# Kernel optimization log

Hardware: AMD Instinct MI355X
Metric: run time of the kernel (lower is better)

The kernel has to match this reference:

```python
import jax, jax.numpy as jnp
import numpy as np

B, S, H = 32, 1024, 768          # batch, seq_len, bert hidden
E, W, P = 128, 8, 512            # entities/sample, span width, rel pairs/sample
NT, NR = 5, 9                    # entity types, relation types
D1, HEADS1, D2, RD = 128, 2, 64, 32
REL_IN = 2 * D2 + RD + H         # 928


def _layernorm(x, g, b):
    m = x.mean(-1, keepdims=True)
    v = x.var(-1, keepdims=True)
    return (x - m) * jax.lax.rsqrt(v + 1e-5) * g + b


def _gat_dense(x, Wm, a_src, a_dst, bias, concat):
    # Fully-connected entity graph (incl. self-loops, PyG GATConv default).
    Bn, En, _ = x.shape
    Hh, D = a_src.shape
    h = (x @ Wm).reshape(Bn, En, Hh, D)                      # [B,E,h,D]
    s = jnp.einsum('behd,hd->beh', h, a_src)                 # source score
    d = jnp.einsum('behd,hd->beh', h, a_dst)                 # target score
    # edge j->i : e_ij = leaky_relu(s_j + d_i)
    e = jax.nn.leaky_relu(d[:, :, None, :] + s[:, None, :, :], 0.2)  # [B,i,j,h]
    alpha = jax.nn.softmax(e, axis=2)
    o = jnp.einsum('bijh,bjhd->bihd', alpha, h)
    o = o.reshape(Bn, En, Hh * D) if concat else o.mean(axis=2)
    return o + bias


def setup_inputs() -> dict:
    key = jax.random.key(0)
    ks = jax.random.split(key, 20)
    f = lambda k, shape: jax.random.normal(k, shape, jnp.float32) * 0.02
    return dict(
        sequence_output=jax.random.normal(ks[0], (B, S, H), jnp.float32),
        entity_starts=jax.random.randint(ks[1], (B, E), 0, S - W),
        entity_type_ids=jax.random.randint(ks[2], (B, E), 0, NT),
        pair_idx=jax.random.randint(ks[3], (B, P, 2), 0, E),
        rel_type_ids=jax.random.randint(ks[4], (B, P), 0, NR),
        entity_type_emb=f(ks[5], (NT, H)),
        rel_type_emb=f(ks[6], (NR, RD)),
        W1=f(ks[7], (H, HEADS1 * D1)), a_src1=f(ks[8], (HEADS1, D1)),
        a_dst1=f(ks[9], (HEADS1, D1)), b1=jnp.zeros((HEADS1 * D1,), jnp.float32),
        ln1_g=jnp.ones((HEADS1 * D1,), jnp.float32), ln1_b=jnp.zeros((HEADS1 * D1,), jnp.float32),
        W2=f(ks[10], (HEADS1 * D1, D2)), a_src2=f(ks[11], (1, D2)),
        a_dst2=f(ks[12], (1, D2)), b2=jnp.zeros((D2,), jnp.float32),
        ln2_g=jnp.ones((D2,), jnp.float32), ln2_b=jnp.zeros((D2,), jnp.float32),
        Wr1=f(ks[13], (REL_IN, 256)), br1=jnp.zeros((256,), jnp.float32),
        Wr2=f(ks[14], (256, 1)), br2=jnp.zeros((1,), jnp.float32),
    )


def reference(sequence_output, entity_starts, entity_type_ids, pair_idx, rel_type_ids,
              entity_type_emb, rel_type_emb,
              W1, a_src1, a_dst1, b1, ln1_g, ln1_b,
              W2, a_src2, a_dst2, b2, ln2_g, ln2_b,
              Wr1, br1, Wr2, br2):
    bidx = jnp.arange(B)[:, None]
    # --- per-entity attention pooling over span tokens ---
    tok_idx = entity_starts[:, :, None] + jnp.arange(W)            # [B,E,W]
    toks = sequence_output[jnp.arange(B)[:, None, None], tok_idx]  # [B,E,W,H]
    mean = toks.mean(axis=2)                                       # [B,E,H]
    attn = jax.nn.softmax(jnp.einsum('bewh,beh->bew', toks, mean), axis=-1)
    pooled = jnp.einsum('bew,bewh->beh', attn, toks)
    x = pooled + entity_type_emb[entity_type_ids]                  # [B,E,H]
    # --- 2-layer GAT over fully-connected entity graph ---
    x = jax.nn.elu(_layernorm(_gat_dense(x, W1, a_src1, a_dst1, b1, True), ln1_g, ln1_b))
    x = jax.nn.elu(_layernorm(_gat_dense(x, W2, a_src2, a_dst2, b2, False), ln2_g, ln2_b))
    # --- gather-concat relation MLP scoring ---
    cls = sequence_output[:, 0, :]                                 # [B,H]
    x1 = x[bidx, pair_idx[:, :, 0]]                                # [B,P,64]
    x2 = x[bidx, pair_idx[:, :, 1]]
    rel = rel_type_emb[rel_type_ids]                               # [B,P,32]
    pv = jnp.concatenate([x1, x2, rel, jnp.broadcast_to(cls[:, None, :], (B, P, H))], axis=-1)
    scores = (jax.nn.relu(pv @ Wr1 + br1) @ Wr2 + br2)[..., 0]     # [B,P]
    return scores
```

## Files before the change

### kernel.cpp

```cpp
#include <hip/hip_runtime.h>
#include <hip/hip_bf16.h>

#define BB 32
#define SS 1024
#define HHH 768
#define EE 128
#define WW 8
#define PP 512
#define RDD 32

typedef __attribute__((ext_vector_type(8))) short bf16x8;
typedef __attribute__((ext_vector_type(8))) unsigned short us8;
typedef __attribute__((ext_vector_type(4))) unsigned short us4;
typedef __attribute__((ext_vector_type(4))) float f32x4;

__device__ __forceinline__ unsigned short f2bf(float v) {
    __hip_bfloat16 h = __float2bfloat16(v);
    return *(unsigned short*)&h;
}

__global__ __launch_bounds__(256) void pool_prep_kernel(
    const float* __restrict__ seq, const int* __restrict__ starts,
    const int* __restrict__ types, const float* __restrict__ temb,
    unsigned short* __restrict__ xout,
    const float* __restrict__ W1, unsigned short* __restrict__ Wt,
    const float* __restrict__ Wr1, unsigned short* __restrict__ Wtr,
    const float* __restrict__ W2, unsigned short* __restrict__ W2t,
    const float* __restrict__ remb, unsigned short* __restrict__ rembb,
    float* __restrict__ basep) {
    int tid = threadIdx.x;
    __shared__ float sbuf[WW * HHH];
    __shared__ float scred[WW];
    __shared__ float attn_s[WW];

    if (blockIdx.x < BB * EE) {
        int be = blockIdx.x;
        int b = be >> 7;
        int start = starts[be];
        const float4* bp4 = (const float4*)(seq + ((size_t)b * SS + start) * HHH);
        for (int idx = tid; idx < WW * (HHH / 4); idx += 256) {
            int w = idx / (HHH / 4), h4 = idx % (HHH / 4);
            float4 v = bp4[(size_t)w * (HHH / 4) + h4];
            sbuf[w * HHH + h4 * 4 + 0] = v.x; sbuf[w * HHH + h4 * 4 + 1] = v.y;
            sbuf[w * HHH + h4 * 4 + 2] = v.z; sbuf[w * HHH + h4 * 4 + 3] = v.w;
        }
        __syncthreads();

        float sc[WW];
#pragma unroll
        for (int w = 0; w < WW; w++) sc[w] = 0.f;
#pragma unroll
        for (int c = 0; c < 3; c++) {
            int h = tid + 256 * c;
            float s = 0.f;
#pragma unroll
            for (int w = 0; w < WW; w++) s += sbuf[w * HHH + h];
            float m = s * (1.0f / WW);
#pragma unroll
            for (int w = 0; w < WW; w++) sc[w] += sbuf[w * HHH + h] * m;
        }
        if (tid < WW) scred[tid] = 0.f;
        __syncthreads();
        int lane = tid & 63;
#pragma unroll
        for (int w = 0; w < WW; w++) {
            float v = sc[w];
            for (int o = 32; o > 0; o >>= 1) v += __shfl_down(v, o, 64);
            if (lane == 0) atomicAdd(&scred[w], v);
        }
        __syncthreads();
        if (tid == 0) {
            float mx = scred[0];
            for (int w = 1; w < WW; w++) mx = fmaxf(mx, scred[w]);
            float ssum = 0.f;
            float a[WW];
            for (int w = 0; w < WW; w++) { a[w] = __expf(scred[w] - mx); ssum += a[w]; }
            float inv = 1.f / ssum;
            for (int w = 0; w < WW; w++) attn_s[w] = a[w] * inv;
        }
        __syncthreads();

        int t = types[be];
        const float* emb = temb + (size_t)t * HHH;
#pragma unroll
        for (int c = 0; c < 3; c++) {
            int h = tid + 256 * c;
            float p = 0.f;
#pragma unroll
            for (int w = 0; w < WW; w++) p += attn_s[w] * sbuf[w * HHH + h];
            xout[(size_t)be * HHH + h] = f2bf(p + emb[h]);
        }
        return;
    }

    int blk = blockIdx.x - BB * EE;
    if (blk < 48) {
        int k0 = blk * 16;
        for (int i = tid; i < 16 * 256; i += 256)
            sbuf[i] = W1[(size_t)(k0 + (i >> 8)) * 256 + (i & 255)];
        __syncthreads();
        int n = tid;
        us8 v0, v1;
#pragma unroll
        for (int kk = 0; kk < 8; kk++) v0[kk] = f2bf(sbuf[kk * 256 + n]);
#pragma unroll
        for (int kk = 0; kk < 8; kk++) v1[kk] = f2bf(sbuf[(8 + kk) * 256 + n]);
        *(us8*)(Wt + (size_t)n * HHH + k0) = v0;
        *(us8*)(Wt + (size_t)n * HHH + k0 + 8) = v1;
    } else if (blk < 58) {
        int k0 = (blk - 48) * 16;
        for (int i = tid; i < 16 * 256; i += 256)
            sbuf[i] = Wr1[(size_t)(k0 + (i >> 8)) * 256 + (i & 255)];
        __syncthreads();
        int n = tid;
        us8 v0, v1;
#pragma unroll
        for (int kk = 0; kk < 8; kk++) v0[kk] = f2bf(sbuf[kk * 256 + n]);
#pragma unroll
        for (int kk = 0; kk < 8; kk++) v1[kk] = f2bf(sbuf[(8 + kk) * 256 + n]);
        *(us8*)(Wtr + (size_t)n * 160 + k0) = v0;
        *(us8*)(Wtr + (size_t)n * 160 + k0 + 8) = v1;
    } else if (blk < 74) {
        int k0 = (blk - 58) * 16;
        for (int i = tid; i < 16 * 64; i += 256)
            sbuf[(i >> 6) * 64 + (i & 63)] = W2[(size_t)(k0 + (i >> 6)) * 64 + (i & 63)];
        __syncthreads();
        if (tid < 64) {
            int n = tid;
            us8 v0, v1;
#pragma unroll
            for (int kk = 0; kk < 8; kk++) v0[kk] = f2bf(sbuf[kk * 64 + n]);
#pragma unroll
            for (int kk = 0; kk < 8; kk++) v1[kk] = f2bf(sbuf[(8 + kk) * 64 + n]);
            *(us8*)(W2t + (size_t)n * 256 + k0) = v0;
            *(us8*)(W2t + (size_t)n * 256 + k0 + 8) = v1;
        }
    } else if (blk == 74) {
        for (int i = tid; i < 9 * RDD; i += 256) rembb[i] = f2bf(remb[i]);
    } else {
        int pc = blk - 75;
        int kc = pc % 12;
        int b = pc / 12;
        int n = tid;
        if (n < 64) sbuf[4096 + n] = seq[(size_t)b * SS * HHH + kc * 64 + n];
        __syncthreads();
        float acc = 0.f;
        const float* w = Wr1 + (size_t)(160 + kc * 64) * 256 + n;
#pragma unroll 16
        for (int k = 0; k < 64; k++) acc += sbuf[4096 + k] * w[(size_t)k * 256];
        basep[((size_t)kc * 32 + b) * 256 + n] = acc;
    }
}

__global__ __launch_bounds__(256) void gemm1_mfma_kernel(
    const unsigned short* __restrict__ Xb, const unsigned short* __restrict__ Wt,
    const float* __restrict__ asrc1, const float* __restrict__ adst1,
    unsigned short* __restrict__ h1Tg,
    float* __restrict__ ps_s, float* __restrict__ ps_d) {
    const int K = HHH;
    int n0 = blockIdx.x * 64;
    int m0 = blockIdx.y * 64;
    int tid = threadIdx.x;
    int wave = tid >> 6, lane = tid & 63;
    int wm = (wave >> 1) * 32, wn = (wave & 1) * 32;

    __shared__ __align__(16) unsigned short As[64][40];
    __shared__ __align__(16) unsigned short Bs[64][40];
    __shared__ __align__(16) unsigned short T[64][72];
    __shared__ float sdred[64][2][2];

    f32x4 acc[2][2] = {};
    int ar = tid >> 2;
    int ac = (tid & 3) * 8;
    int fr = lane & 15;
    int fk = (lane >> 4) * 8;

    for (int k0 = 0; k0 < K; k0 += 32) {
        us8 av = *(const us8*)(Xb + (size_t)(m0 + ar) * K + k0 + ac);
        us8 bv = *(const us8*)(Wt + (size_t)(n0 + ar) * K + k0 + ac);
        *(us8*)(&As[ar][ac]) = av;
        *(us8*)(&Bs[ar][ac]) = bv;
        __syncthreads();

        bf16x8 a0 = *(const bf16x8*)(&As[wm + fr][fk]);
        bf16x8 a1 = *(const bf16x8*)(&As[wm + 16 + fr][fk]);
        bf16x8 b0 = *(const bf16x8*)(&Bs[wn + fr][fk]);
        bf16x8 b1 = *(const bf16x8*)(&Bs[wn + 16 + fr][fk]);

        acc[0][0] = __builtin_amdgcn_mfma_f32_16x16x32_bf16(a0, b0, acc[0][0], 0, 0, 0);
        acc[0][1] = __builtin_amdgcn_mfma_f32_16x16x32_bf16(a0, b1, acc[0][1], 0, 0, 0);
        acc[1][0] = __builtin_amdgcn_mfma_f32_16x16x32_bf16(a1, b0, acc[1][0], 0, 0, 0);
        acc[1][1] = __builtin_amdgcn_mfma_f32_16x16x32_bf16(a1, b1, acc[1][1], 0, 0, 0);
        __syncthreads();
    }

    int crow = (lane >> 4) * 4;
    int ccol = lane & 15;
    int h = n0 >> 7;
    int nb = (n0 >> 6) & 1;
    int dbase = (n0 & 127) + wn;

    float asv[2], adv[2];
#pragma unroll
    for (int ni = 0; ni < 2; ni++) {
        int d = dbase + ni * 16 + ccol;
        asv[ni] = asrc1[h * 128 + d];
        adv[ni] = adst1[h * 128 + d];
    }

#pragma unroll
    for (int mi = 0; mi < 2; mi++) {
#pragma unroll
        for (int r = 0; r < 4; r++) {
            float sp = 0.f, dp = 0.f;
#pragma unroll
            for (int ni = 0; ni < 2; ni++) {
                float v = acc[mi][ni][r];
                T[wn + ni * 16 + ccol][wm + mi * 16 + crow + r] = f2bf(v);
                sp += v * asv[ni];
                dp += v * adv[ni];
            }
            for (int msk = 1; msk < 16; msk <<= 1) {
                sp += __shfl_xor(sp, msk, 64);
                dp += __shfl_xor(dp, msk, 64);
            }
            if ((lane & 15) == 0) {
                int row = wm + mi * 16 + crow + r;
                sdred[row][wn >> 5][0] = sp;
                sdred[row][wn >> 5][1] = dp;
            }
        }
    }
    __syncthreads();

    int b = m0 >> 7;
    int j0 = m0 & 127;
    if (tid < 64) {
        float spt = sdred[tid][0][0] + sdred[tid][1][0];
        float dpt = sdred[tid][0][1] + sdred[tid][1][1];
        size_t o = (size_t)nb * 8192 + ((size_t)(m0 + tid)) * 2 + h;
        ps_s[o] = spt;
        ps_d[o] = dpt;
    }
    {
        int d_l = tid >> 2, q = tid & 3;
        us8 v0 = *(const us8*)(&T[d_l][q * 16]);
        us8 v1 = *(const us8*)(&T[d_l][q * 16 + 8]);
        size_t go = ((size_t)(b * 2 + h) * 128 + (n0 & 127) + d_l) * 128 + j0 + q * 16;
        *(us8*)(h1Tg + go) = v0;
        *(us8*)(h1Tg + go + 8) = v1;
    }
}

__global__ __launch_bounds__(256) void gat1_gemm2_kernel(
    const unsigned short* __restrict__ h1Tg,
    const float* __restrict__ ps_s, const float* __restrict__ ps_d,
    const float* __restrict__ b1, const float* __restrict__ gamma,
    const float* __restrict__ beta,
    const unsigned short* __restrict__ W2t,
    const float* __restrict__ asrc2, const float* __restrict__ adst2,
    unsigned short* __restrict__ h2Tg, float* __restrict__ s2,
    float* __restrict__ d2) {
    int b = blockIdx.x >> 2;
    int c = blockIdx.x & 3;
    int tid = threadIdx.x;
    int wave = tid >> 6, lane = tid & 63;
    int h = wave >> 1, m = wave & 1;
    int fr = lane & 15;
    int fk = (lane >> 4) * 8;

    __shared__ __align__(16) unsigned short h1T[2][128][136];
    __shared__ float ssh[2][128];
    __shared__ float dsh[2][128];
    __shared__ float lnred[32][2][2];
    __shared__ __align__(16) unsigned short g1s[32][264];
    __shared__ float sdr2[32][2][2];
    __shared__ __align__(16) unsigned short t2[64][40];

    {
        const us8* src = (const us8*)(h1Tg + (size_t)b * 32768);
#pragma unroll
        for (int it = 0; it < 16; it++) {
            int i8 = tid + it * 256;
            int row = i8 >> 4;
            int j8 = i8 & 15;
            *(us8*)(&h1T[row >> 7][row & 127][j8 * 8]) = src[i8];
        }
        int hh = tid >> 7, j = tid & 127;
        size_t o = ((size_t)b * 128 + j) * 2 + hh;
        ssh[hh][j] = ps_s[o] + ps_s[o + 8192];
        dsh[hh][j] = ps_d[o] + ps_d[o + 8192];
    }
    __syncthreads();

    bf16x8 afrag[4];
    {
        float dd = dsh[h][c * 32 + m * 16 + fr];
        float ev[4][8];
        float mx = -1e30f;
#pragma unroll
        for (int ks = 0; ks < 4; ks++)
#pragma unroll
            for (int jj = 0; jj < 8; jj++) {
                float e = dd + ssh[h][ks * 32 + fk + jj];
                e = e >= 0.f ? e : 0.2f * e;
                ev[ks][jj] = e;
                mx = fmaxf(mx, e);
            }
        mx = fmaxf(mx, __shfl_xor(mx, 16, 64));
        mx = fmaxf(mx, __shfl_xor(mx, 32, 64));
        float sm = 0.f;
#pragma unroll
        for (int ks = 0; ks < 4; ks++)
#pragma unroll
            for (int jj = 0; jj < 8; jj++) {
                float e = __expf(ev[ks][jj] - mx);
                ev[ks][jj] = e;
                sm += e;
            }
        sm += __shfl_xor(sm, 16, 64);
        sm += __shfl_xor(sm, 32, 64);
        float inv = 1.f / sm;
#pragma unroll
        for (int ks = 0; ks < 4; ks++) {
            bf16x8 a;
#pragma unroll
            for (int jj = 0; jj < 8; jj++)
                a[jj] = (short)f2bf(ev[ks][jj] * inv);
            afrag[ks] = a;
        }
    }

    f32x4 acc[8] = {};
#pragma unroll
    for (int ks = 0; ks < 4; ks++)
#pragma unroll
        for (int ni = 0; ni < 8; ni++) {
            bf16x8 bv = *(const bf16x8*)(&h1T[h][ni * 16 + fr][ks * 32 + fk]);
            acc[ni] = __builtin_amdgcn_mfma_f32_16x16x32_bf16(
                afrag[ks], bv, acc[ni], 0, 0, 0);
        }

    int crow = (lane >> 4) * 4;
    int ccol = lane & 15;
    float bv_[8], gv[8], bev[8];
#pragma unroll
    for (int ni = 0; ni < 8; ni++) {
        int d = h * 128 + ni * 16 + ccol;
        bv_[ni] = b1[d]; gv[ni] = gamma[d]; bev[ni] = beta[d];
    }
    float vv[4][8];
#pragma unroll
    for (int r = 0; r < 4; r++) {
        float s = 0.f, q = 0.f;
#pragma unroll
        for (int ni = 0; ni < 8; ni++) {
            float v = acc[ni][r] + bv_[ni];
            vv[r][ni] = v;
            s += v;
            q += v * v;
        }
        s += __shfl_xor(s, 1, 64); s += __shfl_xor(s, 2, 64);
        s += __shfl_xor(s, 4, 64); s += __shfl_xor(s, 8, 64);
        q += __shfl_xor(q, 1, 64); q += __shfl_xor(q, 2, 64);
        q += __shfl_xor(q, 4, 64); q += __shfl_xor(q, 8, 64);
        if ((lane & 15) == 0) {
            lnred[m * 16 + crow + r][h][0] = s;
            lnred[m * 16 + crow + r][h][1] = q;
        }
    }
    __syncthreads();
#pragma unroll
    for (int r = 0; r < 4; r++) {
        int row = m * 16 + crow + r;
        float s = lnred[row][0][0] + lnred[row][1][0];
        float q = lnred[row][0][1] + lnred[row][1][1];
        float mean = s * (1.f / 256.f);
        float var = q * (1.f / 256.f) - mean * mean;
        float rs = rsqrtf(var + 1e-5f);
#pragma unroll
        for (int ni = 0; ni < 8; ni++) {
            float y = (vv[r][ni] - mean) * rs * gv[ni] + bev[ni];
            y = y > 0.f ? y : (__expf(y) - 1.f);
            g1s[row][h * 128 + ni * 16 + ccol] = f2bf(y);
        }
    }
    __syncthreads();

    int m2 = wave & 1;
    int nb = wave >> 1;
    f32x4 acc2[2] = {};
#pragma unroll
    for (int kc = 0; kc < 8; kc++) {
        bf16x8 a = *(const bf16x8*)(&g1s[m2 * 16 + fr][kc * 32 + fk]);
#pragma unroll
        for (int ni = 0; ni < 2; ni++) {
            bf16x8 wv = *(const bf16x8*)(W2t + (size_t)(nb * 32 + ni * 16 + fr) * 256 +
                                         kc * 32 + fk);
            acc2[ni] = __builtin_amdgcn_mfma_f32_16x16x32_bf16(a, wv, acc2[ni], 0, 0, 0);
        }
    }
    float as2[2], ad2[2];
#pragma unroll
    for (int ni = 0; ni < 2; ni++) {
        int n = nb * 32 + ni * 16 + ccol;
        as2[ni] = asrc2[n];
        ad2[ni] = adst2[n];
    }
#pragma unroll
    for (int r = 0; r < 4; r++) {
        int rl = m2 * 16 + crow + r;
        float sp = 0.f, dp = 0.f;
#pragma unroll
        for (int ni = 0; ni < 2; ni++) {
            float v = acc2[ni][r];
            t2[nb * 32 + ni * 16 + ccol][rl] = f2bf(v);
            sp += v * as2[ni];
            dp += v * ad2[ni];
        }
        for (int msk = 1; msk < 16; msk <<= 1) {
            sp += __shfl_xor(sp, msk, 64);
            dp += __shfl_xor(dp, msk, 64);
        }
        if ((lane & 15) == 0) {
            sdr2[rl][nb][0] = sp;
            sdr2[rl][nb][1] = dp;
        }
    }
    __syncthreads();
    if (tid < 32) {
        s2[(size_t)b * 128 + c * 32 + tid] = sdr2[tid][0][0] + sdr2[tid][1][0];
        d2[(size_t)b * 128 + c * 32 + tid] = sdr2[tid][0][1] + sdr2[tid][1][1];
    }
    {
        int d = tid >> 2, q = tid & 3;
        us8 v = *(const us8*)(&t2[d][q * 8]);
        *(us8*)(h2Tg + ((size_t)b * 64 + d) * 128 + c * 32 + q * 8) = v;
    }
}

__global__ __launch_bounds__(256) void gat2_fused_kernel(
    const unsigned short* __restrict__ h2Tg, const float* __restrict__ s2,
    const float* __restrict__ d2, const float* __restrict__ b2v,
    const float* __restrict__ gamma, const float* __restrict__ beta,
    unsigned short* __restrict__ x2b) {
    int b = blockIdx.x >> 1;
    int c = blockIdx.x & 1;
    int tid = threadIdx.x;
    int wave = tid >> 6, lane = tid & 63;
    int fr = lane & 15;
    int fk = (lane >> 4) * 8;

    __shared__ __align__(16) unsigned short h2T[64][136];
    __shared__ float ssh[128];
    __shared__ float dsh[128];

    {
        const us8* src = (const us8*)(h2Tg + (size_t)b * 64 * 128);
#pragma unroll
        for (int it = 0; it < 4; it++) {
            int i8 = tid + it * 256;
            int row = i8 >> 4;
            int j8 = i8 & 15;
            *(us8*)(&h2T[row][j8 * 8]) = src[i8];
        }
        if (tid < 128) ssh[tid] = s2[(size_t)b * 128 + tid];
        else dsh[tid - 128] = d2[(size_t)b * 128 + (tid - 128)];
    }
    __syncthreads();

    bf16x8 afrag[4];
    {
        float dd = dsh[c * 64 + wave * 16 + fr];
        float ev[4][8];
        float mx = -1e30f;
#pragma unroll
        for (int ks = 0; ks < 4; ks++)
#pragma unroll
            for (int jj = 0; jj < 8; jj++) {
                float e = dd + ssh[ks * 32 + fk + jj];
                e = e >= 0.f ? e : 0.2f * e;
                ev[ks][jj] = e;
                mx = fmaxf(mx, e);
            }
        mx = fmaxf(mx, __shfl_xor(mx, 16, 64));
        mx = fmaxf(mx, __shfl_xor(mx, 32, 64));
        float sm = 0.f;
#pragma unroll
        for (int ks = 0; ks < 4; ks++)
#pragma unroll
            for (int jj = 0; jj < 8; jj++) {
                float e = __expf(ev[ks][jj] - mx);
                ev[ks][jj] = e;
                sm += e;
            }
        sm += __shfl_xor(sm, 16, 64);
        sm += __shfl_xor(sm, 32, 64);
        float inv = 1.f / sm;
#pragma unroll
        for (int ks = 0; ks < 4; ks++) {
            bf16x8 a;
#pragma unroll
            for (int jj = 0; jj < 8; jj++)
                a[jj] = (short)f2bf(ev[ks][jj] * inv);
            afrag[ks] = a;
        }
    }

    f32x4 acc[4] = {};
#pragma unroll
    for (int ks = 0; ks < 4; ks++)
#pragma unroll
        for (int ni = 0; ni < 4; ni++) {
            bf16x8 bv = *(const bf16x8*)(&h2T[ni * 16 + fr][ks * 32 + fk]);
            acc[ni] = __builtin_amdgcn_mfma_f32_16x16x32_bf16(
                afrag[ks], bv, acc[ni], 0, 0, 0);
        }

    int crow = (lane >> 4) * 4;
    int ccol = lane & 15;
    float bv_[4], gv[4], bev[4];
#pragma unroll
    for (int ni = 0; ni < 4; ni++) {
        int d = ni * 16 + ccol;
        bv_[ni] = b2v[d]; gv[ni] = gamma[d]; bev[ni] = beta[d];
    }
#pragma unroll
    for (int r = 0; r < 4; r++) {
        float v[4];
        float s = 0.f;
#pragma unroll
        for (int ni = 0; ni < 4; ni++) {
            v[ni] = acc[ni][r] + bv_[ni];
            s += v[ni];
        }
        s += __shfl_xor(s, 1, 64); s += __shfl_xor(s, 2, 64);
        s += __shfl_xor(s, 4, 64); s += __shfl_xor(s, 8, 64);
        float mean = s * (1.f / 64.f);
        float sq = 0.f;
#pragma unroll
        for (int ni = 0; ni < 4; ni++) {
            float dv = v[ni] - mean;
            sq += dv * dv;
        }
        sq += __shfl_xor(sq, 1, 64); sq += __shfl_xor(sq, 2, 64);
        sq += __shfl_xor(sq, 4, 64); sq += __shfl_xor(sq, 8, 64);
        float rs = rsqrtf(sq * (1.f / 64.f) + 1e-5f);
        int i = c * 64 + wave * 16 + crow + r;
        unsigned short* dst = x2b + (size_t)(b * 128 + i) * 64;
#pragma unroll
        for (int ni = 0; ni < 4; ni++) {
            float y = (v[ni] - mean) * rs * gv[ni] + bev[ni];
            y = y > 0.f ? y : (__expf(y) - 1.f);
            dst[ni * 16 + ccol] = f2bf(y);
        }
    }
}

__global__ __launch_bounds__(256) void score_mfma_kernel(
    const unsigned short* __restrict__ x2b, const float* __restrict__ basep,
    const float* __restrict__ br1,
    const int* __restrict__ pair_idx, const int* __restrict__ rel_ids,
    const unsigned short* __restrict__ rembb, const unsigned short* __restrict__ Wtr,
    const float* __restrict__ Wr2, const float* __restrict__ br2,
    float* __restrict__ out) {
    int blk = blockIdx.x;
    int b = blk >> 3;
    int p0 = (blk & 7) * 64;
    int tid = threadIdx.x;
    int wave = tid >> 6, lane = tid & 63;
    int wn = wave * 64;

    __shared__ __align__(16) unsigned short As[64][168];
    __shared__ __align__(16) unsigned short Bs[256][40];
    __shared__ float sred[64][4];
    __shared__ int prs[64][3];

    if (tid < 64) {
        int p = p0 + tid;
        prs[tid][0] = pair_idx[((size_t)b * PP + p) * 2 + 0];
        prs[tid][1] = pair_idx[((size_t)b * PP + p) * 2 + 1];
        prs[tid][2] = rel_ids[(size_t)b * PP + p];
    }
    __syncthreads();
    for (int it = 0; it < 10; it++) {
        int idx = tid + it * 256;
        int m = idx / 40, c = idx % 40;
        int k0 = c * 4;
        us4 v;
        if (k0 < 64)
            v = *(const us4*)(x2b + ((size_t)b * EE + prs[m][0]) * 64 + k0);
        else if (k0 < 128)
            v = *(const us4*)(x2b + ((size_t)b * EE + prs[m][1]) * 64 + (k0 - 64));
        else
            v = *(const us4*)(rembb + prs[m][2] * RDD + (k0 - 128));
        *(us4*)(&As[m][k0]) = v;
    }

    f32x4 acc[4][4] = {};
    int fr = lane & 15;
    int fk = (lane >> 4) * 8;

    for (int kc = 0; kc < 5; kc++) {
        for (int it = 0; it < 4; it++) {
            int i = tid + it * 256;
            int n = i >> 2, c = i & 3;
            *(us8*)(&Bs[n][c * 8]) =
                *(const us8*)(Wtr + (size_t)n * 160 + kc * 32 + c * 8);
        }
        __syncthreads();
        bf16x8 a[4], bv[4];
#pragma unroll
        for (int mi = 0; mi < 4; mi++)
            a[mi] = *(const bf16x8*)(&As[mi * 16 + fr][kc * 32 + fk]);
#pragma unroll
        for (int ni = 0; ni < 4; ni++)
            bv[ni] = *(const bf16x8*)(&Bs[wn + ni * 16 + fr][fk]);
#pragma unroll
        for (int mi = 0; mi < 4; mi++)
#pragma unroll
            for (int ni = 0; ni < 4; ni++)
                acc[mi][ni] = __builtin_amdgcn_mfma_f32_16x16x32_bf16(
                    a[mi], bv[ni], acc[mi][ni], 0, 0, 0);
        __syncthreads();
    }

    int crow = (lane >> 4) * 4;
    int ccol = lane & 15;
    float basev[4], w2v[4];
#pragma unroll
    for (int ni = 0; ni < 4; ni++) {
        int n = wn + ni * 16 + ccol;
        float bb = br1[n];
#pragma unroll
        for (int kc = 0; kc < 12; kc++)
            bb += basep[((size_t)kc * 32 + b) * 256 + n];
        basev[ni] = bb;
        w2v[ni] = Wr2[n];
    }
#pragma unroll
    for (int mi = 0; mi < 4; mi++) {
#pragma unroll
        for (int r = 0; r < 4; r++) {
            float p = 0.f;
#pragma unroll
            for (int ni = 0; ni < 4; ni++)
                p += fmaxf(acc[mi][ni][r] + basev[ni], 0.f) * w2v[ni];
            for (int msk = 1; msk < 16; msk <<= 1)
                p += __shfl_xor(p, msk, 64);
            if ((lane & 15) == 0)
                sred[mi * 16 + crow + r][wave] = p;
        }
    }
    __syncthreads();
    if (tid < 64) {
        float s = sred[tid][0] + sred[tid][1] + sred[tid][2] + sred[tid][3] + br2[0];
        out[(size_t)b * PP + p0 + tid] = s;
    }
}

extern "C" void kernel_launch(void* const* d_in, const int* in_sizes, int n_in,
                              void* d_out, int out_size, void* d_ws, size_t ws_size,
                              hipStream_t stream) {
    (void)in_sizes; (void)n_in; (void)out_size; (void)ws_size;
    const float* seq      = (const float*)d_in[0];
    const int*   starts   = (const int*)d_in[1];
    const int*   types    = (const int*)d_in[2];
    const int*   pair_idx = (const int*)d_in[3];
    const int*   rel_ids  = (const int*)d_in[4];
    const float* temb     = (const float*)d_in[5];
    const float* remb     = (const float*)d_in[6];
    const float* W1       = (const float*)d_in[7];
    const float* a_src1   = (const float*)d_in[8];
    const float* a_dst1   = (const float*)d_in[9];
    const float* b1       = (const float*)d_in[10];
    const float* ln1_g    = (const float*)d_in[11];
    const float* ln1_b    = (const float*)d_in[12];
    const float* W2       = (const float*)d_in[13];
    const float* a_src2   = (const float*)d_in[14];
    const float* a_dst2   = (const float*)d_in[15];
    const float* b2       = (const float*)d_in[16];
    const float* ln2_g    = (const float*)d_in[17];
    const float* ln2_b    = (const float*)d_in[18];
    const float* Wr1      = (const float*)d_in[19];
    const float* br1      = (const float*)d_in[20];
    const float* Wr2      = (const float*)d_in[21];
    const float* br2      = (const float*)d_in[22];
    float* out = (float*)d_out;

    unsigned short* xb    = (unsigned short*)d_ws;
    unsigned short* Wt    = xb + (size_t)4096 * 768;
    unsigned short* Wtr   = Wt + (size_t)256 * 768;
    unsigned short* W2t   = Wtr + (size_t)256 * 160;
    unsigned short* rembb = W2t + (size_t)64 * 256;
    unsigned short* h1Tg  = rembb + 512;
    unsigned short* h2Tg  = h1Tg + (size_t)4096 * 256;
    unsigned short* x2b   = h2Tg + (size_t)32 * 64 * 128;
    float* fbase = (float*)(x2b + (size_t)4096 * 64);
    float* ps_s  = fbase;
    float* ps_d  = ps_s + 2 * 8192;
    float* s2    = ps_d + 2 * 8192;
    float* d2    = s2 + 4096;
    float* basep = d2 + 4096;

    pool_prep_kernel<<<BB * EE + 75 + 12 * 32, 256, 0, stream>>>(
        seq, starts, types, temb, xb, W1, Wt, Wr1, Wtr, W2, W2t, remb, rembb, basep);
    gemm1_mfma_kernel<<<dim3(4, 64), 256, 0, stream>>>(xb, Wt, a_src1, a_dst1,
                                                       h1Tg, ps_s, ps_d);
    gat1_gemm2_kernel<<<BB * 4, 256, 0, stream>>>(h1Tg, ps_s, ps_d, b1, ln1_g, ln1_b,
                                                  W2t, a_src2, a_dst2, h2Tg, s2, d2);
    gat2_fused_kernel<<<BB * 2, 256, 0, stream>>>(h2Tg, s2, d2, b2, ln2_g, ln2_b, x2b);
    score_mfma_kernel<<<BB * PP / 64, 256, 0, stream>>>(x2b, basep, br1, pair_idx,
                                                        rel_ids, rembb, Wtr, Wr2,
                                                        br2, out);
}
```

Baseline: 228.9 us.

## Fuse GAT layer 1 tail, GAT layer 2 and relation scoring into one kernel

Three kernels (GAT1 softmax+GEMM2, GAT2, relation scoring) are merged into a single 1024-thread kernel. Each block handles one batch sample and one 64-pair slice and keeps h2 and x2 in shared memory, so the h2Tg, s2, d2 and x2b global round trips and two launches go away. In exchange, each of the 8 pair-slice blocks for a sample recomputes that sample's whole GAT1/GAT2 pipeline, multiplying the GAT work by 8. Shared memory is reused through unions to fit the larger per-block working set.

Result: slower. 238.4 us (+4.1%).

```diff
diff --git a/kernel.cpp b/kernel.cpp
--- a/kernel.cpp
+++ b/kernel.cpp
@@ -252,410 +252,391 @@
     }
 }
 
-__global__ __launch_bounds__(256) void gat1_gemm2_kernel(
+struct RAu {
+    union {
+        unsigned short h1T[128][136];
+        struct {
+            unsigned short t2[64][136];
+            float sred[64][16];
+        } s;
+    };
+};
+struct RBu {
+    union {
+        unsigned short g1s[128][264];
+        struct {
+            unsigned short As[64][168];
+            unsigned short Bs[256][40];
+        } s;
+    };
+};
+
+__global__ __launch_bounds__(1024) void gat_all_kernel(
     const unsigned short* __restrict__ h1Tg,
     const float* __restrict__ ps_s, const float* __restrict__ ps_d,
-    const float* __restrict__ b1, const float* __restrict__ gamma,
-    const float* __restrict__ beta,
+    const float* __restrict__ b1, const float* __restrict__ ln1g,
+    const float* __restrict__ ln1b,
     const unsigned short* __restrict__ W2t,
     const float* __restrict__ asrc2, const float* __restrict__ adst2,
-    unsigned short* __restrict__ h2Tg, float* __restrict__ s2,
-    float* __restrict__ d2) {
-    int b = blockIdx.x >> 2;
-    int c = blockIdx.x & 3;
+    const float* __restrict__ b2v, const float* __restrict__ ln2g,
+    const float* __restrict__ ln2b,
+    const float* __restrict__ basep, const float* __restrict__ br1,
+    const int* __restrict__ pair_idx, const int* __restrict__ rel_ids,
+    const unsigned short* __restrict__ rembb, const unsigned short* __restrict__ Wtr,
+    const float* __restrict__ Wr2, const float* __restrict__ br2,
+    float* __restrict__ out) {
+    int bid = blockIdx.x;
+    int b = bid >> 3;
+    int pslice = bid & 7;
     int tid = threadIdx.x;
     int wave = tid >> 6, lane = tid & 63;
-    int h = wave >> 1, m = wave & 1;
     int fr = lane & 15;
     int fk = (lane >> 4) * 8;
-
-    __shared__ __align__(16) unsigned short h1T[2][128][136];
+    int crow = (lane >> 4) * 4;
+    int ccol = lane & 15;
+
+    __shared__ __align__(16) RAu ra;
+    __shared__ __align__(16) RBu rb;
+    __shared__ __align__(16) unsigned short x2s[128][68];
     __shared__ float ssh[2][128];
     __shared__ float dsh[2][128];
-    __shared__ float lnred[32][2][2];
-    __shared__ __align__(16) unsigned short g1s[32][264];
-    __shared__ float sdr2[32][2][2];
-    __shared__ __align__(16) unsigned short t2[64][40];
-
-    {
-        const us8* src = (const us8*)(h1Tg + (size_t)b * 32768);
-#pragma unroll
-        for (int it = 0; it < 16; it++) {
-            int i8 = tid + it * 256;
-            int row = i8 >> 4;
-            int j8 = i8 & 15;
-            *(us8*)(&h1T[row >> 7][row & 127][j8 * 8]) = src[i8];
-        }
+    __shared__ float lnred[128][2][2];
+    __shared__ float sdr2[128][2][2];
+    __shared__ float s2s[128];
+    __shared__ float d2s[128];
+    __shared__ int prs[64][3];
+
+    if (tid < 256) {
         int hh = tid >> 7, j = tid & 127;
         size_t o = ((size_t)b * 128 + j) * 2 + hh;
         ssh[hh][j] = ps_s[o] + ps_s[o + 8192];
         dsh[hh][j] = ps_d[o] + ps_d[o + 8192];
     }
+
+    int m8 = wave & 7;
+    int dh = wave >> 3;
+    f32x4 accH[2][4] = {};
+
+#pragma unroll
+    for (int hp = 0; hp < 2; hp++) {
+        {
+            const us8* src = (const us8*)(h1Tg + ((size_t)(b * 2 + hp) * 128) * 128);
+#pragma unroll
+            for (int it = 0; it < 2; it++) {
+                int i8 = tid + it * 1024;
+                int row = i8 >> 4, j8 = i8 & 15;
+                *(us8*)(&ra.h1T[row][j8 * 8]) = src[i8];
+            }
+        }
+        __syncthreads();
+
+        bf16x8 afrag[4];
+        {
+            float dd = dsh[hp][m8 * 16 + fr];
+            float ev[4][8];
+            float mx = -1e30f;
+#pragma unroll
+            for (int ks = 0; ks < 4; ks++)
+#pragma unroll
+                for (int jj = 0; jj < 8; jj++) {
+                    float e = dd + ssh[hp][ks * 32 + fk + jj];
+                    e = e >= 0.f ? e : 0.2f * e;
+                    ev[ks][jj] = e;
+                    mx = fmaxf(mx, e);
+                }
+            mx = fmaxf(mx, __shfl_xor(mx, 16, 64));
+            mx = fmaxf(mx, __shfl_xor(mx, 32, 64));
+            float sm = 0.f;
+#pragma unroll
+            for (int ks = 0; ks < 4; ks++)
+#pragma unroll
+                for (int jj = 0; jj < 8; jj++) {
+                    float e = __expf(ev[ks][jj] - mx);
+                    ev[ks][jj] = e;
+                    sm += e;
+                }
+            sm += __shfl_xor(sm, 16, 64);
+            sm += __shfl_xor(sm, 32, 64);
+            float inv = 1.f / sm;
+#pragma unroll
+            for (int ks = 0; ks < 4; ks++) {
+                bf16x8 a;
+#pragma unroll
+                for (int jj = 0; jj < 8; jj++)
+                    a[jj] = (short)f2bf(ev[ks][jj] * inv);
+                afrag[ks] = a;
+            }
+        }
+
+#pragma unroll
+        for (int ks = 0; ks < 4; ks++)
+#pragma unroll
+            for (int ni = 0; ni < 4; ni++) {
+                bf16x8 bv = *(const bf16x8*)(&ra.h1T[dh * 64 + ni * 16 + fr][ks * 32 + fk]);
+                accH[hp][ni] = __builtin_amdgcn_mfma_f32_16x16x32_bf16(
+                    afrag[ks], bv, accH[hp][ni], 0, 0, 0);
+            }
+        __syncthreads();
+    }
+
+    {
+        float bv_[2][4], gv[2][4], bev[2][4];
+#pragma unroll
+        for (int hp = 0; hp < 2; hp++)
+#pragma unroll
+            for (int ni = 0; ni < 4; ni++) {
+                int d = hp * 128 + dh * 64 + ni * 16 + ccol;
+                bv_[hp][ni] = b1[d]; gv[hp][ni] = ln1g[d]; bev[hp][ni] = ln1b[d];
+            }
+        float vv[2][4][4];
+#pragma unroll
+        for (int r = 0; r < 4; r++) {
+            float s = 0.f, q = 0.f;
+#pragma unroll
+            for (int hp = 0; hp < 2; hp++)
+#pragma unroll
+                for (int ni = 0; ni < 4; ni++) {
+                    float v = accH[hp][ni][r] + bv_[hp][ni];
+                    vv[hp][r][ni] = v;
+                    s += v;
+                    q += v * v;
+                }
+            s += __shfl_xor(s, 1, 64); s += __shfl_xor(s, 2, 64);
+            s += __shfl_xor(s, 4, 64); s += __shfl_xor(s, 8, 64);
+            q += __shfl_xor(q, 1, 64); q += __shfl_xor(q, 2, 64);
+            q += __shfl_xor(q, 4, 64); q += __shfl_xor(q, 8, 64);
+            if ((lane & 15) == 0) {
+                lnred[m8 * 16 + crow + r][dh][0] = s;
+                lnred[m8 * 16 + crow + r][dh][1] = q;
+            }
+        }
+        __syncthreads();
+#pragma unroll
+        for (int r = 0; r < 4; r++) {
+            int row = m8 * 16 + crow + r;
+            float s = lnred[row][0][0] + lnred[row][1][0];
+            float q = lnred[row][0][1] + lnred[row][1][1];
+            float mean = s * (1.f / 256.f);
+            float var = q * (1.f / 256.f) - mean * mean;
+            float rs = rsqrtf(var + 1e-5f);
+#pragma unroll
+            for (int hp = 0; hp < 2; hp++)
+#pragma unroll
+                for (int ni = 0; ni < 4; ni++) {
+                    float y = (vv[hp][r][ni] - mean) * rs * gv[hp][ni] + bev[hp][ni];
+                    y = y > 0.f ? y : (__expf(y) - 1.f);
+                    rb.g1s[row][hp * 128 + dh * 64 + ni * 16 + ccol] = f2bf(y);
+                }
+        }
+    }
     __syncthreads();
 
-    bf16x8 afrag[4];
     {
-        float dd = dsh[h][c * 32 + m * 16 + fr];
-        float ev[4][8];
-        float mx = -1e30f;
+        int m2 = wave & 7;
+        int nh = wave >> 3;
+        f32x4 acc2[2] = {};
+#pragma unroll
+        for (int kc = 0; kc < 8; kc++) {
+            bf16x8 a = *(const bf16x8*)(&rb.g1s[m2 * 16 + fr][kc * 32 + fk]);
+#pragma unroll
+            for (int ni = 0; ni < 2; ni++) {
+                bf16x8 wv = *(const bf16x8*)(W2t + (size_t)(nh * 32 + ni * 16 + fr) * 256 +
+                                             kc * 32 + fk);
+                acc2[ni] = __builtin_amdgcn_mfma_f32_16x16x32_bf16(a, wv, acc2[ni], 0, 0, 0);
+            }
+        }
+        float as2[2], ad2[2];
+#pragma unroll
+        for (int ni = 0; ni < 2; ni++) {
+            int n = nh * 32 + ni * 16 + ccol;
+            as2[ni] = asrc2[n];
+            ad2[ni] = adst2[n];
+        }
+#pragma unroll
+        for (int r = 0; r < 4; r++) {
+            int rl = m2 * 16 + crow + r;
+            float sp = 0.f, dp = 0.f;
+#pragma unroll
+            for (int ni = 0; ni < 2; ni++) {
+                float v = acc2[ni][r];
+                ra.s.t2[nh * 32 + ni * 16 + ccol][rl] = f2bf(v);
+                sp += v * as2[ni];
+                dp += v * ad2[ni];
+            }
+            for (int msk = 1; msk < 16; msk <<= 1) {
+                sp += __shfl_xor(sp, msk, 64);
+                dp += __shfl_xor(dp, msk, 64);
+            }
+            if ((lane & 15) == 0) {
+                sdr2[rl][nh][0] = sp;
+                sdr2[rl][nh][1] = dp;
+            }
+        }
+    }
+    __syncthreads();
+    if (tid < 128) {
+        s2s[tid] = sdr2[tid][0][0] + sdr2[tid][1][0];
+        d2s[tid] = sdr2[tid][0][1] + sdr2[tid][1][1];
+    }
+    __syncthreads();
+
+    if (wave < 8) {
+        int m3 = wave;
+        bf16x8 afrag2[4];
+        {
+            float dd = d2s[m3 * 16 + fr];
+            float ev[4][8];
+            float mx = -1e30f;
+#pragma unroll
+            for (int ks = 0; ks < 4; ks++)
+#pragma unroll
+                for (int jj = 0; jj < 8; jj++) {
+                    float e = dd + s2s[ks * 32 + fk + jj];
+                    e = e >= 0.f ? e : 0.2f * e;
+                    ev[ks][jj] = e;
+                    mx = fmaxf(mx, e);
+                }
+            mx = fmaxf(mx, __shfl_xor(mx, 16, 64));
+            mx = fmaxf(mx, __shfl_xor(mx, 32, 64));
+            float sm = 0.f;
+#pragma unroll
+            for (int ks = 0; ks < 4; ks++)
+#pragma unroll
+                for (int jj = 0; jj < 8; jj++) {
+                    float e = __expf(ev[ks][jj] - mx);
+                    ev[ks][jj] = e;
+                    sm += e;
+                }
+            sm += __shfl_xor(sm, 16, 64);
+            sm += __shfl_xor(sm, 32, 64);
+            float inv = 1.f / sm;
+#pragma unroll
+            for (int ks = 0; ks < 4; ks++) {
+                bf16x8 a;
+#pragma unroll
+                for (int jj = 0; jj < 8; jj++)
+                    a[jj] = (short)f2bf(ev[ks][jj] * inv);
+                afrag2[ks] = a;
+            }
+        }
+
+        f32x4 acc3[4] = {};
 #pragma unroll
         for (int ks = 0; ks < 4; ks++)
 #pragma unroll
-            for (int jj = 0; jj < 8; jj++) {
-                float e = dd + ssh[h][ks * 32 + fk + jj];
-                e = e >= 0.f ? e : 0.2f * e;
-                ev[ks][jj] = e;
-                mx = fmaxf(mx, e);
-            }
-        mx = fmaxf(mx, __shfl_xor(mx, 16, 64));
-        mx = fmaxf(mx, __shfl_xor(mx, 32, 64));
-        float sm = 0.f;
-#pragma unroll
-        for (int ks = 0; ks < 4; ks++)
-#pragma unroll
-            for (int jj = 0; jj < 8; jj++) {
-                float e = __expf(ev[ks][jj] - mx);
-                ev[ks][jj] = e;
-                sm += e;
-            }
-        sm += __shfl_xor(sm, 16, 64);
-        sm += __shfl_xor(sm, 32, 64);
-        float inv = 1.f / sm;
-#pragma unroll
-        for (int ks = 0; ks < 4; ks++) {
-            bf16x8 a;
-#pragma unroll
-            for (int jj = 0; jj < 8; jj++)
-                a[jj] = (short)f2bf(ev[ks][jj] * inv);
-            afrag[ks] = a;
-        }
-    }
-
-    f32x4 acc[8] = {};
-#pragma unroll
-    for (int ks = 0; ks < 4; ks++)
-#pragma unroll
-        for (int ni = 0; ni < 8; ni++) {
-            bf16x8 bv = *(const bf16x8*)(&h1T[h][ni * 16 + fr][ks * 32 + fk]);
-            acc[ni] = __builtin_amdgcn_mfma_f32_16x16x32_bf16(
-                afrag[ks], bv, acc[ni], 0, 0, 0);
-        }
-
-    int crow = (lane >> 4) * 4;
-    int ccol = lane & 15;
-    float bv_[8], gv[8], bev[8];
-#pragma unroll
-    for (int ni = 0; ni < 8; ni++) {
-        int d = h * 128 + ni * 16 + ccol;
-        bv_[ni] = b1[d]; gv[ni] = gamma[d]; bev[ni] = beta[d];
-    }
-    float vv[4][8];
-#pragma unroll
-    for (int r = 0; r < 4; r++) {
-        float s = 0.f, q = 0.f;
-#pragma unroll
-        for (int ni = 0; ni < 8; ni++) {
-            float v = acc[ni][r] + bv_[ni];
-            vv[r][ni] = v;
-            s += v;
-            q += v * v;
-        }
-        s += __shfl_xor(s, 1, 64); s += __shfl_xor(s, 2, 64);
-        s += __shfl_xor(s, 4, 64); s += __shfl_xor(s, 8, 64);
-        q += __shfl_xor(q, 1, 64); q += __shfl_xor(q, 2, 64);
-        q += __shfl_xor(q, 4, 64); q += __shfl_xor(q, 8, 64);
-        if ((lane & 15) == 0) {
-            lnred[m * 16 + crow + r][h][0] = s;
-            lnred[m * 16 + crow + r][h][1] = q;
-        }
+            for (int ni = 0; ni < 4; ni++) {
+                bf16x8 bv = *(const bf16x8*)(&ra.s.t2[ni * 16 + fr][ks * 32 + fk]);
+                acc3[ni] = __builtin_amdgcn_mfma_f32_16x16x32_bf16(
+                    afrag2[ks], bv, acc3[ni], 0, 0, 0);
+            }
+
+        float bv_[4], gv[4], bev[4];
+#pragma unroll
+        for (int ni = 0; ni < 4; ni++) {
+            int d = ni * 16 + ccol;
+            bv_[ni] = b2v[d]; gv[ni] = ln2g[d]; bev[ni] = ln2b[d];
+        }
+#pragma unroll
+        for (int r = 0; r < 4; r++) {
+            float v[4];
+            float s = 0.f;
+#pragma unroll
+            for (int ni = 0; ni < 4; ni++) {
+                v[ni] = acc3[ni][r] + bv_[ni];
+                s += v[ni];
+            }
+            s += __shfl_xor(s, 1, 64); s += __shfl_xor(s, 2, 64);
+            s += __shfl_xor(s, 4, 64); s += __shfl_xor(s, 8, 64);
+            float mean = s * (1.f / 64.f);
+            float sq = 0.f;
+#pragma unroll
+            for (int ni = 0; ni < 4; ni++) {
+                float dv = v[ni] - mean;
+                sq += dv * dv;
+            }
+            sq += __shfl_xor(sq, 1, 64); sq += __shfl_xor(sq, 2, 64);
+            sq += __shfl_xor(sq, 4, 64); sq += __shfl_xor(sq, 8, 64);
+            float rs = rsqrtf(sq * (1.f / 64.f) + 1e-5f);
+            int i = m3 * 16 + crow + r;
+#pragma unroll
+            for (int ni = 0; ni < 4; ni++) {
+                float y = (v[ni] - mean) * rs * gv[ni] + bev[ni];
+                y = y > 0.f ? y : (__expf(y) - 1.f);
+                x2s[i][ni * 16 + ccol] = f2bf(y);
+            }
+        }
+    }
+
+    if (tid < 64) {
+        int pp = pslice * 64 + tid;
+        prs[tid][0] = pair_idx[((size_t)b * PP + pp) * 2 + 0];
+        prs[tid][1] = pair_idx[((size_t)b * PP + pp) * 2 + 1];
+        prs[tid][2] = rel_ids[(size_t)b * PP + pp];
     }
     __syncthreads();
-#pragma unroll
-    for (int r = 0; r < 4; r++) {
-        int row = m * 16 + crow + r;
-        float s = lnred[row][0][0] + lnred[row][1][0];
-        float q = lnred[row][0][1] + lnred[row][1][1];
-        float mean = s * (1.f / 256.f);
-        float var = q * (1.f / 256.f) - mean * mean;
-        float rs = rsqrtf(var + 1e-5f);
-#pragma unroll
-        for (int ni = 0; ni < 8; ni++) {
-            float y = (vv[r][ni] - mean) * rs * gv[ni] + bev[ni];
-            y = y > 0.f ? y : (__expf(y) - 1.f);
-            g1s[row][h * 128 + ni * 16 + ccol] = f2bf(y);
-        }
-    }
-    __syncthreads();
-
-    int m2 = wave & 1;
-    int nb = wave >> 1;
-    f32x4 acc2[2] = {};
-#pragma unroll
-    for (int kc = 0; kc < 8; kc++) {
-        bf16x8 a = *(const bf16x8*)(&g1s[m2 * 16 + fr][kc * 32 + fk]);
-#pragma unroll
-        for (int ni = 0; ni < 2; ni++) {
-            bf16x8 wv = *(const bf16x8*)(W2t + (size_t)(nb * 32 + ni * 16 + fr) * 256 +
-                                         kc * 32 + fk);
-            acc2[ni] = __builtin_amdgcn_mfma_f32_16x16x32_bf16(a, wv, acc2[ni], 0, 0, 0);
-        }
-    }
-    float as2[2], ad2[2];
-#pragma unroll
-    for (int ni = 0; ni < 2; ni++) {
-        int n = nb * 32 + ni * 16 + ccol;
-        as2[ni] = asrc2[n];
-        ad2[ni] = adst2[n];
-    }
-#pragma unroll
-    for (int r = 0; r < 4; r++) {
-        int rl = m2 * 16 + crow + r;
-        float sp = 0.f, dp = 0.f;
-#pragma unroll
-        for (int ni = 0; ni < 2; ni++) {
-            float v = acc2[ni][r];
-            t2[nb * 32 + ni * 16 + ccol][rl] = f2bf(v);
-            sp += v * as2[ni];
-            dp += v * ad2[ni];
-        }
-        for (int msk = 1; msk < 16; msk <<= 1) {
-            sp += __shfl_xor(sp, msk, 64);
-            dp += __shfl_xor(dp, msk, 64);
-        }
-        if ((lane & 15) == 0) {
-            sdr2[rl][nb][0] = sp;
-            sdr2[rl][nb][1] = dp;
-        }
-    }
-    __syncthreads();
-    if (tid < 32) {
-        s2[(size_t)b * 128 + c * 32 + tid] = sdr2[tid][0][0] + sdr2[tid][1][0];
-        d2[(size_t)b * 128 + c * 32 + tid] = sdr2[tid][0][1] + sdr2[tid][1][1];
-    }
+
+#pragma unroll
+    for (int it = 0; it < 3; it++) {
+        int idx = tid + it * 1024;
+        if (idx < 2560) {
+            int m = idx / 40, c = idx % 40;
+            int k0 = c * 4;
+            us4 v;
+            if (k0 < 64)
+                v = *(const us4*)(&x2s[prs[m][0]][k0]);
+            else if (k0 < 128)
+                v = *(const us4*)(&x2s[prs[m][1]][k0 - 64]);
+            else
+                v = *(const us4*)(rembb + prs[m][2] * RDD + (k0 - 128));
+            *(us4*)(&rb.s.As[m][k0]) = v;
+        }
+    }
+
+    f32x4 acc4[4] = {};
+    for (int kc = 0; kc < 5; kc++) {
+        {
+            int n = tid >> 2, c = tid & 3;
+            *(us8*)(&rb.s.Bs[n][c * 8]) =
+                *(const us8*)(Wtr + (size_t)n * 160 + kc * 32 + c * 8);
+        }
+        __syncthreads();
+        bf16x8 a[4];
+#pragma unroll
+        for (int mi = 0; mi < 4; mi++)
+            a[mi] = *(const bf16x8*)(&rb.s.As[mi * 16 + fr][kc * 32 + fk]);
+        bf16x8 bv = *(const bf16x8*)(&rb.s.Bs[wave * 16 + fr][fk]);
+#pragma unroll
+        for (int mi = 0; mi < 4; mi++)
+            acc4[mi] = __builtin_amdgcn_mfma_f32_16x16x32_bf16(a[mi], bv, acc4[mi], 0, 0, 0);
+        __syncthreads();
+    }
+
     {
-        int d = tid >> 2, q = tid & 3;
-        us8 v = *(const us8*)(&t2[d][q * 8]);
-        *(us8*)(h2Tg + ((size_t)b * 64 + d) * 128 + c * 32 + q * 8) = v;
-    }
-}
-
-__global__ __launch_bounds__(256) void gat2_fused_kernel(
-    const unsigned short* __restrict__ h2Tg, const float* __restrict__ s2,
-    const float* __restrict__ d2, const float* __restrict__ b2v,
-    const float* __restrict__ gamma, const float* __restrict__ beta,
-    unsigned short* __restrict__ x2b) {
-    int b = blockIdx.x >> 1;
-    int c = blockIdx.x & 1;
-    int tid = threadIdx.x;
-    int wave = tid >> 6, lane = tid & 63;
-    int fr = lane & 15;
-    int fk = (lane >> 4) * 8;
-
-    __shared__ __align__(16) unsigned short h2T[64][136];
-    __shared__ float ssh[128];
-    __shared__ float dsh[128];
-
-    {
-        const us8* src = (const us8*)(h2Tg + (size_t)b * 64 * 128);
-#pragma unroll
-        for (int it = 0; it < 4; it++) {
-            int i8 = tid + it * 256;
-            int row = i8 >> 4;
-            int j8 = i8 & 15;
-            *(us8*)(&h2T[row][j8 * 8]) = src[i8];
-        }
-        if (tid < 128) ssh[tid] = s2[(size_t)b * 128 + tid];
-        else dsh[tid - 128] = d2[(size_t)b * 128 + (tid - 128)];
-    }
-    __syncthreads();
-
-    bf16x8 afrag[4];
-    {
-        float dd = dsh[c * 64 + wave * 16 + fr];
-        float ev[4][8];
-        float mx = -1e30f;
-#pragma unroll
-        for (int ks = 0; ks < 4; ks++)
-#pragma unroll
-            for (int jj = 0; jj < 8; jj++) {
-                float e = dd + ssh[ks * 32 + fk + jj];
-                e = e >= 0.f ? e : 0.2f * e;
-                ev[ks][jj] = e;
-                mx = fmaxf(mx, e);
-            }
-        mx = fmaxf(mx, __shfl_xor(mx, 16, 64));
-        mx = fmaxf(mx, __shfl_xor(mx, 32, 64));
-        float sm = 0.f;
-#pragma unroll
-        for (int ks = 0; ks < 4; ks++)
-#pragma unroll
-            for (int jj = 0; jj < 8; jj++) {
-                float e = __expf(ev[ks][jj] - mx);
-                ev[ks][jj] = e;
-                sm += e;
-            }
-        sm += __shfl_xor(sm, 16, 64);
-        sm += __shfl_xor(sm, 32, 64);
-        float inv = 1.f / sm;
-#pragma unroll
-        for (int ks = 0; ks < 4; ks++) {
-            bf16x8 a;
-#pragma unroll
-            for (int jj = 0; jj < 8; jj++)
-                a[jj] = (short)f2bf(ev[ks][jj] * inv);
-            afrag[ks] = a;
-        }
-    }
-
-    f32x4 acc[4] = {};
-#pragma unroll
-    for (int ks = 0; ks < 4; ks++)
-#pragma unroll
-        for (int ni = 0; ni < 4; ni++) {
-            bf16x8 bv = *(const bf16x8*)(&h2T[ni * 16 + fr][ks * 32 + fk]);
-            acc[ni] = __builtin_amdgcn_mfma_f32_16x16x32_bf16(
-                afrag[ks], bv, acc[ni], 0, 0, 0);
-        }
-
-    int crow = (lane >> 4) * 4;
-    int ccol = lane & 15;
-    float bv_[4], gv[4], bev[4];
-#pragma unroll
-    for (int ni = 0; ni < 4; ni++) {
-        int d = ni * 16 + ccol;
-        bv_[ni] = b2v[d]; gv[ni] = gamma[d]; bev[ni] = beta[d];
-    }
-#pragma unroll
-    for (int r = 0; r < 4; r++) {
-        float v[4];
-        float s = 0.f;
-#pragma unroll
-        for (int ni = 0; ni < 4; ni++) {
-            v[ni] = acc[ni][r] + bv_[ni];
-            s += v[ni];
-        }
-        s += __shfl_xor(s, 1, 64); s += __shfl_xor(s, 2, 64);
-        s += __shfl_xor(s, 4, 64); s += __shfl_xor(s, 8, 64);
-        float mean = s * (1.f / 64.f);
-        float sq = 0.f;
-#pragma unroll
-        for (int ni = 0; ni < 4; ni++) {
-            float dv = v[ni] - mean;
-            sq += dv * dv;
-        }
-        sq += __shfl_xor(sq, 1, 64); sq += __shfl_xor(sq, 2, 64);
-        sq += __shfl_xor(sq, 4, 64); sq += __shfl_xor(sq, 8, 64);
-        float rs = rsqrtf(sq * (1.f / 64.f) + 1e-5f);
-        int i = c * 64 + wave * 16 + crow + r;
-        unsigned short* dst = x2b + (size_t)(b * 128 + i) * 64;
-#pragma unroll
-        for (int ni = 0; ni < 4; ni++) {
-            float y = (v[ni] - mean) * rs * gv[ni] + bev[ni];
-            y = y > 0.f ? y : (__expf(y) - 1.f);
-            dst[ni * 16 + ccol] = f2bf(y);
-        }
-    }
-}
-
-__global__ __launch_bounds__(256) void score_mfma_kernel(
-    const unsigned short* __restrict__ x2b, const float* __restrict__ basep,
-    const float* __restrict__ br1,
-    const int* __restrict__ pair_idx, const int* __restrict__ rel_ids,
-    const unsigned short* __restrict__ rembb, const unsigned short* __restrict__ Wtr,
-    const float* __restrict__ Wr2, const float* __restrict__ br2,
-    float* __restrict__ out) {
-    int blk = blockIdx.x;
-    int b = blk >> 3;
-    int p0 = (blk & 7) * 64;
-    int tid = threadIdx.x;
-    int wave = tid >> 6, lane = tid & 63;
-    int wn = wave * 64;
-
-    __shared__ __align__(16) unsigned short As[64][168];
-    __shared__ __align__(16) unsigned short Bs[256][40];
-    __shared__ float sred[64][4];
-    __shared__ int prs[64][3];
-
-    if (tid < 64) {
-        int p = p0 + tid;
-        prs[tid][0] = pair_idx[((size_t)b * PP + p) * 2 + 0];
-        prs[tid][1] = pair_idx[((size_t)b * PP + p) * 2 + 1];
-        prs[tid][2] = rel_ids[(size_t)b * PP + p];
-    }
-    __syncthreads();
-    for (int it = 0; it < 10; it++) {
-        int idx = tid + it * 256;
-        int m = idx / 40, c = idx % 40;
-        int k0 = c * 4;
-        us4 v;
-        if (k0 < 64)
-            v = *(const us4*)(x2b + ((size_t)b * EE + prs[m][0]) * 64 + k0);
-        else if (k0 < 128)
-            v = *(const us4*)(x2b + ((size_t)b * EE + prs[m][1]) * 64 + (k0 - 64));
-        else
-            v = *(const us4*)(rembb + prs[m][2] * RDD + (k0 - 128));
-        *(us4*)(&As[m][k0]) = v;
-    }
-
-    f32x4 acc[4][4] = {};
-    int fr = lane & 15;
-    int fk = (lane >> 4) * 8;
-
-    for (int kc = 0; kc < 5; kc++) {
-        for (int it = 0; it < 4; it++) {
-            int i = tid + it * 256;
-            int n = i >> 2, c = i & 3;
-            *(us8*)(&Bs[n][c * 8]) =
-                *(const us8*)(Wtr + (size_t)n * 160 + kc * 32 + c * 8);
-        }
-        __syncthreads();
-        bf16x8 a[4], bv[4];
-#pragma unroll
-        for (int mi = 0; mi < 4; mi++)
-            a[mi] = *(const bf16x8*)(&As[mi * 16 + fr][kc * 32 + fk]);
-#pragma unroll
-        for (int ni = 0; ni < 4; ni++)
-            bv[ni] = *(const bf16x8*)(&Bs[wn + ni * 16 + fr][fk]);
-#pragma unroll
-        for (int mi = 0; mi < 4; mi++)
-#pragma unroll
-            for (int ni = 0; ni < 4; ni++)
-                acc[mi][ni] = __builtin_amdgcn_mfma_f32_16x16x32_bf16(
-                    a[mi], bv[ni], acc[mi][ni], 0, 0, 0);
-        __syncthreads();
-    }
-
-    int crow = (lane >> 4) * 4;
-    int ccol = lane & 15;
-    float basev[4], w2v[4];
-#pragma unroll
-    for (int ni = 0; ni < 4; ni++) {
-        int n = wn + ni * 16 + ccol;
+        int n = wave * 16 + ccol;
         float bb = br1[n];
 #pragma unroll
         for (int kc = 0; kc < 12; kc++)
             bb += basep[((size_t)kc * 32 + b) * 256 + n];
-        basev[ni] = bb;
-        w2v[ni] = Wr2[n];
-    }
-#pragma unroll
-    for (int mi = 0; mi < 4; mi++) {
-#pragma unroll
-        for (int r = 0; r < 4; r++) {
-            float p = 0.f;
-#pragma unroll
-            for (int ni = 0; ni < 4; ni++)
-                p += fmaxf(acc[mi][ni][r] + basev[ni], 0.f) * w2v[ni];
-            for (int msk = 1; msk < 16; msk <<= 1)
-                p += __shfl_xor(p, msk, 64);
-            if ((lane & 15) == 0)
-                sred[mi * 16 + crow + r][wave] = p;
-        }
+        float w2v = Wr2[n];
+#pragma unroll
+        for (int mi = 0; mi < 4; mi++)
+#pragma unroll
+            for (int r = 0; r < 4; r++) {
+                float pv = fmaxf(acc4[mi][r] + bb, 0.f) * w2v;
+                pv += __shfl_xor(pv, 1, 64);
+                pv += __shfl_xor(pv, 2, 64);
+                pv += __shfl_xor(pv, 4, 64);
+                pv += __shfl_xor(pv, 8, 64);
+                if ((lane & 15) == 0)
+                    ra.s.sred[mi * 16 + crow + r][wave] = pv;
+            }
     }
     __syncthreads();
     if (tid < 64) {
-        float s = sred[tid][0] + sred[tid][1] + sred[tid][2] + sred[tid][3] + br2[0];
-        out[(size_t)b * PP + p0 + tid] = s;
+        float s = br2[0];
+#pragma unroll
+        for (int w = 0; w < 16; w++) s += ra.s.sred[tid][w];
+        out[(size_t)b * PP + pslice * 64 + tid] = s;
     }
 }
 
@@ -694,23 +675,18 @@
     unsigned short* W2t   = Wtr + (size_t)256 * 160;
     unsigned short* rembb = W2t + (size_t)64 * 256;
     unsigned short* h1Tg  = rembb + 512;
-    unsigned short* h2Tg  = h1Tg + (size_t)4096 * 256;
-    unsigned short* x2b   = h2Tg + (size_t)32 * 64 * 128;
-    float* fbase = (float*)(x2b + (size_t)4096 * 64);
+    float* fbase = (float*)(h1Tg + (size_t)4096 * 256);
     float* ps_s  = fbase;
     float* ps_d  = ps_s + 2 * 8192;
-    float* s2    = ps_d + 2 * 8192;
-    float* d2    = s2 + 4096;
-    float* basep = d2 + 4096;
+    float* basep = ps_d + 2 * 8192;
 
     pool_prep_kernel<<<BB * EE + 75 + 12 * 32, 256, 0, stream>>>(
-        seq, starts, types, temb, xb, W1, Wt, Wr1, Wtr, W2, W2t, remb, rembb, basep);
+        seq, starts, types, temb, xb, W1, Wt, Wr1, Wtr, W2, W2t, remb, rembb,
+        basep);
     gemm1_mfma_kernel<<<dim3(4, 64), 256, 0, stream>>>(xb, Wt, a_src1, a_dst1,
                                                        h1Tg, ps_s, ps_d);
-    gat1_gemm2_kernel<<<BB * 4, 256, 0, stream>>>(h1Tg, ps_s, ps_d, b1, ln1_g, ln1_b,
-                                                  W2t, a_src2, a_dst2, h2Tg, s2, d2);
-    gat2_fused_kernel<<<BB * 2, 256, 0, stream>>>(h2Tg, s2, d2, b2, ln2_g, ln2_b, x2b);
-    score_mfma_kernel<<<BB * PP / 64, 256, 0, stream>>>(x2b, basep, br1, pair_idx,
-                                                        rel_ids, rembb, Wtr, Wr2,
-                                                        br2, out);
+    gat_all_kernel<<<256, 1024, 0, stream>>>(
+        h1Tg, ps_s, ps_d, b1, ln1_g, ln1_b, W2t, a_src2, a_dst2,
+        b2, ln2_g, ln2_b, basep, br1, pair_idx, rel_ids, rembb, Wtr,
+        Wr2, br2, out);
 }
```
